# Kernel tuning notes

Measured on AMD Instinct MI355X. Metric: run time of the kernel, lower is better.

## Reference

```python
import jax, jax.numpy as jnp
import numpy as np

B, C, H, W = 2, 14, 128, 128
LOSS_WEIGHT = 0.5  # output = (1 - loss_weight) * sum of per-(bs,cls) log-Hausdorff losses
BIG = 1e6          # 'infinite' 1D distance for columns with no background pixel


def _edt_sq(is_zero):
    """Exact squared Euclidean distance transform of a [H,W] bool map.

    Returns, for every pixel, the squared distance to the nearest True pixel
    of `is_zero` (0 at True pixels). Matches scipy.ndimage.distance_transform_edt
    squared. Two-phase separable brute force (vectorized, no data loops).
    """
    h, w = is_zero.shape
    ii = jnp.arange(h, dtype=jnp.float32)
    absd = jnp.abs(ii[:, None] - ii[None, :])  # [H(i), H(p)] = |i - p|
    # d1[i, q] = min_{p : is_zero[p, q]} |i - p|   (per-column 1D distance)
    d1 = jnp.min(jnp.where(is_zero[None, :, :], absd[:, :, None], BIG), axis=1)  # [H, W]
    jj = jnp.arange(w, dtype=jnp.float32)
    off = (jj[:, None] - jj[None, :]) ** 2  # [W(q), W(j)] = (q - j)^2
    # sq[i, j] = min_q d1[i, q]^2 + (q - j)^2
    return jnp.min(d1[:, :, None] ** 2 + off[None, :, :], axis=1)  # [H, W]


def _distance_field_sq(img):
    """MONAI HausdorffDTLoss.distance_field squared: (edt(fg)+edt(bg))^2.

    fg_dist and bg_dist have disjoint supports, so (fg+bg)^2 = fg^2 + bg^2.
    Zero field if the image is all-foreground or all-background.
    """
    fg = img > 0.5
    field = _edt_sq(~fg) + _edt_sq(fg)
    valid = jnp.any(fg) & jnp.any(~fg)
    return jnp.where(valid, field, 0.0)


def _edge_mask(m):
    """mask XOR binary_erosion(mask): scipy default cross structuring element,
    border_value=0 (borders erode)."""
    p = jnp.pad(m, 1, constant_values=False)
    er = m & p[:-2, 1:-1] & p[2:, 1:-1] & p[1:-1, :-2] & p[1:-1, 2:]
    return m & ~er


def _pair_loss(stud_logit, seg_s, seg_t, teach_pred):
    # stud_logit: [H,W] float logits of this class; seg_s/seg_t: [H,W] bool
    # class masks; teach_pred: [H,W] teacher argmax labels (int)
    es = _edge_mask(seg_s).astype(stud_logit.dtype)
    et = _edge_mask(seg_t)
    pred = es * stud_logit                                      # edges * logits
    targ = jnp.where(et, teach_pred.astype(stud_logit.dtype), 0.0)  # edges * labels
    pred_dt2 = jax.lax.stop_gradient(_distance_field_sq(pred))  # MONAI detaches dt
    targ_dt2 = jax.lax.stop_gradient(_distance_field_sq(targ))
    hd = jnp.mean((pred - targ) ** 2 * (pred_dt2 + targ_dt2))   # alpha = 2
    return jnp.log(hd + 1.0)                                    # LogHausdorffDTLoss


def reference(logits_student, logits_teacher):
    ps = jnp.argmax(logits_student, axis=1)  # softmax is monotone -> argmax of logits
    pt = jnp.argmax(logits_teacher, axis=1)
    cls = jnp.arange(1, C)                   # classes 1..C-1 (background skipped)
    n = B * (C - 1)
    seg_s = (ps[:, None] == cls[None, :, None, None]).reshape(n, H, W)
    seg_t = (pt[:, None] == cls[None, :, None, None]).reshape(n, H, W)
    stud = logits_student[:, 1:].reshape(n, H, W)
    pt_rep = jnp.broadcast_to(pt[:, None], (B, C - 1, H, W)).reshape(n, H, W)
    losses = jax.vmap(_pair_loss)(stud, seg_s, seg_t, pt_rep)
    return (1.0 - LOSS_WEIGHT) * jnp.sum(losses)


def setup_inputs() -> dict:
    key = jax.random.key(0)
    k1, k2 = jax.random.split(key)
    return {
        "logits_student": jax.random.normal(k1, (B, C, H, W), dtype=jnp.float32),
        "logits_teacher": jax.random.normal(k2, (B, C, H, W), dtype=jnp.float32),
    }
```

## Files before the change

### kernel.cpp

```cpp
#include <hip/hip_runtime.h>
#include <math.h>
#include <limits.h>

#define HH 128
#define WW 128
#define HW (HH*WW)
#define BB 2
#define CC 14
#define NPAIR 26
#define RPB 4
#define NBLK (NPAIR * (HH / RPB))

typedef unsigned long long u64;


__device__ inline int nbd(u64 lo, u64 hi, int i) {
    int up = 255, down = 255;
    u64 slo, shi;
    if (i == 0)      { slo = lo; shi = hi; }
    else if (i < 64) { slo = (lo >> i) | (hi << (64 - i)); shi = hi >> i; }
    else             { slo = hi >> (i - 64); shi = 0ULL; }
    if (slo)      up = __builtin_ctzll(slo);
    else if (shi) up = 64 + __builtin_ctzll(shi);
    int s = 127 - i;
    u64 llo, lhi;
    if (s == 0)      { llo = lo; lhi = hi; }
    else if (s < 64) { lhi = (hi << s) | (lo >> (64 - s)); llo = lo << s; }
    else             { lhi = lo << (s - 64); llo = 0ULL; }
    if (lhi)      down = __builtin_clzll(lhi);
    else if (llo) down = 64 + __builtin_clzll(llo);
    return min(up, down);
}

__global__ void k_argmax(const float* __restrict__ Ls, const float* __restrict__ Lt,
                         unsigned char* __restrict__ ps, unsigned char* __restrict__ pt,
                         int* __restrict__ flags, float* __restrict__ sums,
                         int* __restrict__ done) {
    if (blockIdx.x == 0) {
        if (threadIdx.x < NPAIR) { flags[threadIdx.x] = 0; sums[threadIdx.x] = 0.0f; }
        if (threadIdx.x == 0) *done = 0;
    }
    int tid = blockIdx.x * blockDim.x + threadIdx.x;
    const int total4 = BB * HW / 4;
    if (tid >= 2 * total4) return;
    const float* L; unsigned char* dst; int p4;
    if (tid < total4) { L = Ls; dst = ps; p4 = tid; }
    else              { L = Lt; dst = pt; p4 = tid - total4; }
    int b = p4 / (HW / 4);
    int q4 = p4 - b * (HW / 4);
    const float4* base = (const float4*)(L + (size_t)b * CC * HW) + q4;
    float4 best = base[0];
    uchar4 bi = make_uchar4(0, 0, 0, 0);
#pragma unroll
    for (int c = 1; c < CC; ++c) {
        float4 v = base[(size_t)c * (HW / 4)];
        if (v.x > best.x) { best.x = v.x; bi.x = (unsigned char)c; }
        if (v.y > best.y) { best.y = v.y; bi.y = (unsigned char)c; }
        if (v.z > best.z) { best.z = v.z; bi.z = (unsigned char)c; }
        if (v.w > best.w) { best.w = v.w; bi.w = (unsigned char)c; }
    }
    ((uchar4*)dst)[b * (HW / 4) + q4] = bi;
}

__device__ inline u64 asm64(unsigned int (*p)[WW], int k0, int j) {
    return (u64)p[k0][j] | ((u64)p[k0 + 1][j] << 16)
         | ((u64)p[k0 + 2][j] << 32) | ((u64)p[k0 + 3][j] << 48);
}

__global__ __launch_bounds__(1024) void k_prep(
        const unsigned char* __restrict__ ps, const unsigned char* __restrict__ pt,
        const float* __restrict__ Ls,
        ulonglong2* __restrict__ cbP, ulonglong2* __restrict__ cbT,
        ulonglong2* __restrict__ esC, int* __restrict__ flags) {
    int n = blockIdx.x;
    int tid = threadIdx.x;
    int k = tid >> 7;
    int j = tid & (WW - 1);
    int b = n / (CC - 1), c = 1 + (n - b * (CC - 1));
    const unsigned char* P = ps + b * HW;
    const unsigned char* T = pt + b * HW;
    const float* Lp = Ls + (size_t)(b * CC + c) * HW;

    unsigned int s16 = 0, t16 = 0, h16 = 0;
    int i0 = k << 4;
#pragma unroll
    for (int r = 0; r < 16; ++r) {
        int off = (i0 + r) * WW + j;
        if (P[off] == c)      s16 |= 1u << r;
        if (T[off] == c)      t16 |= 1u << r;
        if (Lp[off] > 0.5f)   h16 |= 1u << r;
    }
    __shared__ unsigned int pS[8][WW], pT[8][WW], pH[8][WW];
    pS[k][j] = s16; pT[k][j] = t16; pH[k][j] = h16;
    __syncthreads();

    if (tid < WW) {
        u64 ms0 = asm64(pS, 0, j), ms1 = asm64(pS, 4, j);
        u64 mt0 = asm64(pT, 0, j), mt1 = asm64(pT, 4, j);
        u64 hi0 = asm64(pH, 0, j), hi1 = asm64(pH, 4, j);
        u64 Lsx = 0, Lsy = 0, Ltx = 0, Lty = 0, Rsx = 0, Rsy = 0, Rtx = 0, Rty = 0;
        if (j > 0)      { Lsx = asm64(pS, 0, j - 1); Lsy = asm64(pS, 4, j - 1);
                          Ltx = asm64(pT, 0, j - 1); Lty = asm64(pT, 4, j - 1); }
        if (j < WW - 1) { Rsx = asm64(pS, 0, j + 1); Rsy = asm64(pS, 4, j + 1);
                          Rtx = asm64(pT, 0, j + 1); Rty = asm64(pT, 4, j + 1); }

        u64 U0 = ms0 << 1, U1 = (ms1 << 1) | (ms0 >> 63);
        u64 D0 = (ms0 >> 1) | (ms1 << 63), D1 = ms1 >> 1;
        u64 er0 = ms0 & U0 & D0 & Lsx & Rsx;
        u64 er1 = ms1 & U1 & D1 & Lsy & Rsy;
        u64 es0 = ms0 & ~er0, es1 = ms1 & ~er1;

        u64 Ut0 = mt0 << 1, Ut1 = (mt1 << 1) | (mt0 >> 63);
        u64 Dt0 = (mt0 >> 1) | (mt1 << 63), Dt1 = mt1 >> 1;
        u64 ert0 = mt0 & Ut0 & Dt0 & Ltx & Rtx;
        u64 ert1 = mt1 & Ut1 & Dt1 & Lty & Rty;
        u64 et0 = mt0 & ~ert0, et1 = mt1 & ~ert1;

        u64 fp0 = es0 & hi0, fp1 = es1 & hi1;

        int idx = n * WW + j;
        cbP[idx] = make_ulonglong2(fp0, fp1);
        cbT[idx] = make_ulonglong2(et0, et1);
        esC[idx] = make_ulonglong2(es0, es1);

        u64 bFgP = __ballot((fp0 | fp1) != 0ull);
        u64 bBgP = __ballot((fp0 & fp1) != ~0ull);
        u64 bFgT = __ballot((et0 | et1) != 0ull);
        u64 bBgT = __ballot((et0 & et1) != ~0ull);
        if ((j & 63) == 0) {
            int fl = (bFgP ? 1 : 0) | (bBgP ? 2 : 0) | (bFgT ? 4 : 0) | (bBgT ? 8 : 0);
            atomicOr(&flags[n], fl);
        }
    }
}

__global__ __launch_bounds__(512) void k_C(
        const float* __restrict__ Ls,
        const ulonglong2* __restrict__ cbP, const ulonglong2* __restrict__ cbT,
        const ulonglong2* __restrict__ esC,
        const int* __restrict__ flags, float* __restrict__ sums,
        int* __restrict__ done, float* __restrict__ out) {
    int n = blockIdx.x >> 5;
    int t = blockIdx.x & 31;
    int r = threadIdx.x >> 7;
    int j = threadIdx.x & (WW - 1);
    int i = t * RPB + r;
    int b = n / (CC - 1), c = 1 + (n - b * (CC - 1));

    int idx = n * WW + j;
    ulonglong2 mP = cbP[idx];
    ulonglong2 mT = cbT[idx];
    ulonglong2 eS = esC[idx];
    int f = flags[n];
    bool aP = (f & 3) == 3, aT = (f & 12) == 12;

    int dP  = nbd(mP.x, mP.y, i);
    int dPb = nbd(~mP.x, ~mP.y, i);
    int dT  = nbd(mT.x, mT.y, i);
    int dTb = nbd(~mT.x, ~mT.y, i);

    __shared__ ushort4 sq[RPB][WW];
    sq[r][j] = make_ushort4((unsigned short)(dP * dP), (unsigned short)(dPb * dPb),
                            (unsigned short)(dT * dT), (unsigned short)(dTb * dTb));
    __syncthreads();

    int bP = dP * dP, bPb = dPb * dPb, bT = dT * dT, bTb = dTb * dTb;
    int need = 0;
    if (aP) need = max(bP, bPb);
    if (aT) need = max(need, max(bT, bTb));
    for (int rad = 1; rad < WW; ++rad) {
        int rr = rad * rad;
        if (rr >= need) break;
        if (j >= rad) {
            ushort4 s = sq[r][j - rad];
            bP  = min(bP,  (int)s.x + rr); bPb = min(bPb, (int)s.y + rr);
            bT  = min(bT,  (int)s.z + rr); bTb = min(bTb, (int)s.w + rr);
        }
        if (j + rad < WW) {
            ushort4 s = sq[r][j + rad];
            bP  = min(bP,  (int)s.x + rr); bPb = min(bPb, (int)s.y + rr);
            bT  = min(bT,  (int)s.z + rr); bTb = min(bTb, (int)s.w + rr);
        }
        need = 0;
        if (aP) need = max(bP, bPb);
        if (aT) need = max(need, max(bT, bTb));
    }

    float fieldP = aP ? (float)(bP + bPb) : 0.0f;
    float fieldT = aT ? (float)(bT + bTb) : 0.0f;

    bool es = ((i < 64 ? (eS.x >> i) : (eS.y >> (i - 64))) & 1ull) != 0;
    bool et = ((i < 64 ? (mT.x >> i) : (mT.y >> (i - 64))) & 1ull) != 0;
    float lv = Ls[(size_t)(b * CC + c) * HW + i * WW + j];
    float predv = es ? lv : 0.0f;
    float targv = et ? (float)c : 0.0f;
    float diff = predv - targv;
    float v = diff * diff * (fieldP + fieldT);

    for (int o = 32; o > 0; o >>= 1) v += __shfl_down(v, o);
    __shared__ float wsum[8];
    __shared__ int won;
    int lane = threadIdx.x & 63, w = threadIdx.x >> 6;
    if (lane == 0) wsum[w] = v;
    if (threadIdx.x == 0) won = 0;
    __syncthreads();
    if (threadIdx.x == 0) {
        float tot = 0.0f;
#pragma unroll
        for (int k = 0; k < 8; ++k) tot += wsum[k];
        atomicAdd(&sums[n], tot);
        __threadfence();
        if (atomicAdd(done, 1) == NBLK - 1) won = 1;
    }
    __syncthreads();
    if (won && threadIdx.x < 64) {
        float vv = 0.0f;
        if (threadIdx.x < NPAIR) {
            float hd = atomicAdd(&sums[threadIdx.x], 0.0f) * (1.0f / (float)HW);
            vv = logf(hd + 1.0f);
        }
        for (int o = 32; o > 0; o >>= 1) vv += __shfl_down(vv, o);
        if (threadIdx.x == 0) out[0] = 0.5f * vv;
    }
}

extern "C" void kernel_launch(void* const* d_in, const int* in_sizes, int n_in,
                              void* d_out, int out_size, void* d_ws, size_t ws_size,
                              hipStream_t stream) {
    const float* Ls = (const float*)d_in[0];
    const float* Lt = (const float*)d_in[1];
    float* out = (float*)d_out;

    char* w = (char*)d_ws;
    unsigned char* ps    = (unsigned char*)(w);
    unsigned char* pt    = (unsigned char*)(w + 32768);
    ulonglong2*    cbP   = (ulonglong2*)   (w + 65536);
    ulonglong2*    cbT   = (ulonglong2*)   (w + 118784);
    ulonglong2*    esC   = (ulonglong2*)   (w + 172032);
    int*           flags = (int*)          (w + 225280);
    float*         sums  = (float*)        (w + 225408);
    int*           done  = (int*)          (w + 225536);

    k_argmax<<<(2 * BB * HW / 4 + 255) / 256, 256, 0, stream>>>(Ls, Lt, ps, pt, flags, sums, done);
    k_prep<<<NPAIR, 1024, 0, stream>>>(ps, pt, Ls, cbP, cbT, esC, flags);
    k_C<<<NBLK, 512, 0, stream>>>(Ls, cbP, cbT, esC, flags, sums, done, out);
}
```

Before: 79.44 us.

## Fuse argmax into prep kernel and shrink row-distance shared buffer to bytes

Removes the separate argmax kernel and its byte label buffers. Each prep block now computes, per pixel, whether its class wins the argmax by comparing the class logit against all 14 channels of both student and teacher, with tie-breaking that matches first-index argmax. This drops one kernel launch and a global round trip, but each of the 26 blocks rereads all channels, so global loads rise roughly 13-fold and run on only 26 blocks. The flag atomics are replaced by a shared-memory combine, and the EDT shared buffer stores raw 1D distances as uchar4 that are squared on read, halving shared traffic at the cost of extra multiplies.

```diff
diff --git a/kernel.cpp b/kernel.cpp
--- a/kernel.cpp
+++ b/kernel.cpp
@@ -32,65 +32,53 @@
     return min(up, down);
 }
 
-__global__ void k_argmax(const float* __restrict__ Ls, const float* __restrict__ Lt,
-                         unsigned char* __restrict__ ps, unsigned char* __restrict__ pt,
-                         int* __restrict__ flags, float* __restrict__ sums,
-                         int* __restrict__ done) {
-    if (blockIdx.x == 0) {
-        if (threadIdx.x < NPAIR) { flags[threadIdx.x] = 0; sums[threadIdx.x] = 0.0f; }
-        if (threadIdx.x == 0) *done = 0;
-    }
-    int tid = blockIdx.x * blockDim.x + threadIdx.x;
-    const int total4 = BB * HW / 4;
-    if (tid >= 2 * total4) return;
-    const float* L; unsigned char* dst; int p4;
-    if (tid < total4) { L = Ls; dst = ps; p4 = tid; }
-    else              { L = Lt; dst = pt; p4 = tid - total4; }
-    int b = p4 / (HW / 4);
-    int q4 = p4 - b * (HW / 4);
-    const float4* base = (const float4*)(L + (size_t)b * CC * HW) + q4;
-    float4 best = base[0];
-    uchar4 bi = make_uchar4(0, 0, 0, 0);
-#pragma unroll
-    for (int c = 1; c < CC; ++c) {
-        float4 v = base[(size_t)c * (HW / 4)];
-        if (v.x > best.x) { best.x = v.x; bi.x = (unsigned char)c; }
-        if (v.y > best.y) { best.y = v.y; bi.y = (unsigned char)c; }
-        if (v.z > best.z) { best.z = v.z; bi.z = (unsigned char)c; }
-        if (v.w > best.w) { best.w = v.w; bi.w = (unsigned char)c; }
-    }
-    ((uchar4*)dst)[b * (HW / 4) + q4] = bi;
-}
-
 __device__ inline u64 asm64(unsigned int (*p)[WW], int k0, int j) {
     return (u64)p[k0][j] | ((u64)p[k0 + 1][j] << 16)
          | ((u64)p[k0 + 2][j] << 32) | ((u64)p[k0 + 3][j] << 48);
 }
 
 __global__ __launch_bounds__(1024) void k_prep(
-        const unsigned char* __restrict__ ps, const unsigned char* __restrict__ pt,
-        const float* __restrict__ Ls,
+        const float* __restrict__ Ls, const float* __restrict__ Lt,
         ulonglong2* __restrict__ cbP, ulonglong2* __restrict__ cbT,
-        ulonglong2* __restrict__ esC, int* __restrict__ flags) {
+        ulonglong2* __restrict__ esC, int* __restrict__ flags,
+        float* __restrict__ sums, int* __restrict__ done) {
     int n = blockIdx.x;
     int tid = threadIdx.x;
     int k = tid >> 7;
     int j = tid & (WW - 1);
     int b = n / (CC - 1), c = 1 + (n - b * (CC - 1));
-    const unsigned char* P = ps + b * HW;
-    const unsigned char* T = pt + b * HW;
-    const float* Lp = Ls + (size_t)(b * CC + c) * HW;
+    if (tid == 0) { sums[n] = 0.0f; if (n == 0) *done = 0; }
+
+    const float* S = Ls + (size_t)b * CC * HW;
+    const float* T = Lt + (size_t)b * CC * HW;
 
     unsigned int s16 = 0, t16 = 0, h16 = 0;
     int i0 = k << 4;
-#pragma unroll
+#pragma unroll 4
     for (int r = 0; r < 16; ++r) {
         int off = (i0 + r) * WW + j;
-        if (P[off] == c)      s16 |= 1u << r;
-        if (T[off] == c)      t16 |= 1u << r;
-        if (Lp[off] > 0.5f)   h16 |= 1u << r;
+        float vc = S[(size_t)c * HW + off];
+        bool is = true;
+#pragma unroll
+        for (int ch = 0; ch < CC; ++ch) {
+            if (ch == c) continue;
+            float v = S[(size_t)ch * HW + off];
+            is = is && (ch < c ? (vc > v) : (vc >= v));
+        }
+        float wc = T[(size_t)c * HW + off];
+        bool it = true;
+#pragma unroll
+        for (int ch = 0; ch < CC; ++ch) {
+            if (ch == c) continue;
+            float v = T[(size_t)ch * HW + off];
+            it = it && (ch < c ? (wc > v) : (wc >= v));
+        }
+        if (is)          s16 |= 1u << r;
+        if (it)          t16 |= 1u << r;
+        if (vc > 0.5f)   h16 |= 1u << r;
     }
     __shared__ unsigned int pS[8][WW], pT[8][WW], pH[8][WW];
+    __shared__ int sfl[2];
     pS[k][j] = s16; pT[k][j] = t16; pH[k][j] = h16;
     __syncthreads();
 
@@ -127,11 +115,13 @@
         u64 bBgP = __ballot((fp0 & fp1) != ~0ull);
         u64 bFgT = __ballot((et0 | et1) != 0ull);
         u64 bBgT = __ballot((et0 & et1) != ~0ull);
-        if ((j & 63) == 0) {
-            int fl = (bFgP ? 1 : 0) | (bBgP ? 2 : 0) | (bFgT ? 4 : 0) | (bBgT ? 8 : 0);
-            atomicOr(&flags[n], fl);
-        }
-    }
+        if ((tid & 63) == 0) {
+            sfl[tid >> 6] = (bFgP ? 1 : 0) | (bBgP ? 2 : 0)
+                          | (bFgT ? 4 : 0) | (bBgT ? 8 : 0);
+        }
+    }
+    __syncthreads();
+    if (tid == 0) flags[n] = sfl[0] | sfl[1];
 }
 
 __global__ __launch_bounds__(512) void k_C(
@@ -159,9 +149,9 @@
     int dT  = nbd(mT.x, mT.y, i);
     int dTb = nbd(~mT.x, ~mT.y, i);
 
-    __shared__ ushort4 sq[RPB][WW];
-    sq[r][j] = make_ushort4((unsigned short)(dP * dP), (unsigned short)(dPb * dPb),
-                            (unsigned short)(dT * dT), (unsigned short)(dTb * dTb));
+    __shared__ uchar4 sq[RPB][WW];
+    sq[r][j] = make_uchar4((unsigned char)dP, (unsigned char)dPb,
+                           (unsigned char)dT, (unsigned char)dTb);
     __syncthreads();
 
     int bP = dP * dP, bPb = dPb * dPb, bT = dT * dT, bTb = dTb * dTb;
@@ -172,14 +162,14 @@
         int rr = rad * rad;
         if (rr >= need) break;
         if (j >= rad) {
-            ushort4 s = sq[r][j - rad];
-            bP  = min(bP,  (int)s.x + rr); bPb = min(bPb, (int)s.y + rr);
-            bT  = min(bT,  (int)s.z + rr); bTb = min(bTb, (int)s.w + rr);
+            uchar4 s = sq[r][j - rad];
+            bP  = min(bP,  (int)s.x * s.x + rr); bPb = min(bPb, (int)s.y * s.y + rr);
+            bT  = min(bT,  (int)s.z * s.z + rr); bTb = min(bTb, (int)s.w * s.w + rr);
         }
         if (j + rad < WW) {
-            ushort4 s = sq[r][j + rad];
-            bP  = min(bP,  (int)s.x + rr); bPb = min(bPb, (int)s.y + rr);
-            bT  = min(bT,  (int)s.z + rr); bTb = min(bTb, (int)s.w + rr);
+            uchar4 s = sq[r][j + rad];
+            bP  = min(bP,  (int)s.x * s.x + rr); bPb = min(bPb, (int)s.y * s.y + rr);
+            bT  = min(bT,  (int)s.z * s.z + rr); bTb = min(bTb, (int)s.w * s.w + rr);
         }
         need = 0;
         if (aP) need = max(bP, bPb);
@@ -207,7 +197,7 @@
     if (threadIdx.x == 0) {
         float tot = 0.0f;
 #pragma unroll
-        for (int k = 0; k < 8; ++k) tot += wsum[k];
+        for (int q = 0; q < 8; ++q) tot += wsum[q];
         atomicAdd(&sums[n], tot);
         __threadfence();
         if (atomicAdd(done, 1) == NBLK - 1) won = 1;
@@ -232,16 +222,13 @@
     float* out = (float*)d_out;
 
     char* w = (char*)d_ws;
-    unsigned char* ps    = (unsigned char*)(w);
-    unsigned char* pt    = (unsigned char*)(w + 32768);
-    ulonglong2*    cbP   = (ulonglong2*)   (w + 65536);
-    ulonglong2*    cbT   = (ulonglong2*)   (w + 118784);
-    ulonglong2*    esC   = (ulonglong2*)   (w + 172032);
-    int*           flags = (int*)          (w + 225280);
-    float*         sums  = (float*)        (w + 225408);
-    int*           done  = (int*)          (w + 225536);
-
-    k_argmax<<<(2 * BB * HW / 4 + 255) / 256, 256, 0, stream>>>(Ls, Lt, ps, pt, flags, sums, done);
-    k_prep<<<NPAIR, 1024, 0, stream>>>(ps, pt, Ls, cbP, cbT, esC, flags);
+    ulonglong2*    cbP   = (ulonglong2*)(w);
+    ulonglong2*    cbT   = (ulonglong2*)(w + 53248);
+    ulonglong2*    esC   = (ulonglong2*)(w + 106496);
+    int*           flags = (int*)       (w + 159744);
+    float*         sums  = (float*)     (w + 159872);
+    int*           done  = (int*)       (w + 160000);
+
+    k_prep<<<NPAIR, 1024, 0, stream>>>(Ls, Lt, cbP, cbT, esC, flags, sums, done);
     k_C<<<NBLK, 512, 0, stream>>>(Ls, cbP, cbT, esC, flags, sums, done, out);
 }
```

Result: slower. 218.7 us (+175.4%).
